# Kernel tuning notes

Measured on AMD Instinct MI355X. Metric: run time of the kernel, lower is better.

## Reference

```python
import jax, jax.numpy as jnp
import numpy as np
from jax import lax

K_SIZE = 3
STRIDE = 1
PADDING = 1


def setup_inputs() -> dict:
    key = jax.random.key(0)
    k1, k2, k3 = jax.random.split(key, 3)
    x = jax.random.normal(k1, (4, 64, 64, 256), dtype=jnp.float32)
    # small offsets so bilinear sampling stays near the regular grid (realistic DCN behavior)
    offset_w = jax.random.normal(k2, (3, 3, 256, 27), dtype=jnp.float32) * 0.01
    offset_b = jnp.zeros((1, 1, 1, 27), dtype=jnp.float32)
    dcn_weight = jax.random.normal(k3, (256, 256, 3, 3), dtype=jnp.float32) * 0.02
    return {"x": x, "offset_w": offset_w, "offset_b": offset_b, "dcn_weight": dcn_weight}


def _dcnv2(x, offset_w, offset_b, dcn_weight):
    k, stride, padding = K_SIZE, STRIDE, PADDING
    N, H, W, C = x.shape
    kk = k * k
    # offset/mask prediction conv (stride=1 -> SAME padding, per original code)
    om = lax.conv_general_dilated(
        x, offset_w, window_strides=(stride, stride), padding='SAME',
        dimension_numbers=('NHWC', 'HWIO', 'NHWC')) + offset_b
    offset = om[..., : 2 * kk]                      # [N,oH,oW,2k^2] (y,x) pairs
    mask = jax.nn.sigmoid(om[..., 2 * kk:])         # [N,oH,oW,k^2]
    oH = (H + 2 * padding - (k - 1)) // stride
    oW = (W + 2 * padding - (k - 1)) // stride
    # asymmetric zero padding ((p, p+1), (p, p+1)) as in the original
    pad_x = jnp.pad(x, ((0, 0), (padding, padding + 1), (padding, padding + 1), (0, 0)))
    # sampling grid: base center + fixed kernel offsets + learned offsets
    base_y = jnp.arange(oH, dtype=x.dtype) * stride + padding   # [oH]
    base_x = jnp.arange(oW, dtype=x.dtype) * stride + padding   # [oW]
    kr = jnp.arange(k, dtype=x.dtype) - (k - 1) / 2.0
    inner_y = jnp.repeat(kr, k)   # [k^2], row-major (kH, kW)
    inner_x = jnp.tile(kr, k)
    off_yx = offset.reshape(N, oH, oW, kk, 2)
    pos_y = base_y[None, :, None, None] + inner_y[None, None, None, :] + off_yx[..., 0]
    pos_x = base_x[None, None, :, None] + inner_x[None, None, None, :] + off_yx[..., 1]
    pos_y = jnp.clip(pos_y, 0.0, H + 2 * padding - 1.0)
    pos_x = jnp.clip(pos_x, 0.0, W + 2 * padding - 1.0)
    y1 = jnp.floor(pos_y)
    x1 = jnp.floor(pos_x)
    y1i = y1.astype(jnp.int32)
    x1i = x1.astype(jnp.int32)
    y2i = y1i + 1
    x2i = x1i + 1
    gather = jax.vmap(lambda px, yi, xi: px[yi, xi])  # per-sample [oH,oW,k^2] -> [oH,oW,k^2,C]
    v1 = gather(pad_x, y1i, x1i)
    v2 = gather(pad_x, y1i, x2i)
    v3 = gather(pad_x, y2i, x1i)
    v4 = gather(pad_x, y2i, x2i)
    lh = (pos_y - y1)[..., None]
    lw = (pos_x - x1)[..., None]
    hh = 1.0 - lh
    hw = 1.0 - lw
    value = (hh * hw * v1 + hh * lw * v2 + lh * hw * v3 + lh * lw * v4) * mask[..., None]
    # [N,oH,oW,k^2,C] -> [N,oH,oW,C,k^2] -> [N,oH,oW,C*k^2], matching original layout
    value = jnp.transpose(value, (0, 1, 2, 4, 3)).reshape(N, oH, oW, C * kk)
    w = jnp.transpose(dcn_weight, (1, 2, 3, 0)).reshape(C * kk, -1)  # [C*k^2, out_C]
    return jnp.einsum('nhwc,cf->nhwf', value, w)


def reference(x, offset_w, offset_b, dcn_weight):
    return _dcnv2(x, offset_w, offset_b, dcn_weight)
```

## Files before the change

kernel.cpp:

```cpp
#include <hip/hip_runtime.h>
#include <hip/hip_fp16.h>
#include <math.h>

typedef __attribute__((ext_vector_type(8))) _Float16 f16x8;
typedef __attribute__((ext_vector_type(4))) float f32x4;

#define XP_OFF   0
#define XP_BYTES (4*67*67*256*2)
#define WT_OFF   XP_BYTES
#define WT_BYTES (2304*256*2)
#define WOT_OFF  (WT_OFF + WT_BYTES)
#define WOT_BYTES (2304*32*2)
#define OM_OFF   (WOT_OFF + WOT_BYTES)
#define OM_BYTES (16384*32*4)
#define V_OFF    (OM_OFF + OM_BYTES)
#define V_BYTES  ((size_t)16384*2304*2)
#define WS_NEED  ((size_t)V_OFF + V_BYTES)

#define AS1(p) ((const __attribute__((address_space(1))) void*)(p))
#define AS3(p) ((__attribute__((address_space(3))) void*)(p))

__global__ __launch_bounds__(256) void prep_all(const float* __restrict__ x,
        const float* __restrict__ dw, const float* __restrict__ ow,
        __half* __restrict__ xp, __half* __restrict__ wt, __half* __restrict__ wot) {
    int b = blockIdx.x, tid = threadIdx.x;
    if (b < 2245) {
        int g = b * 256 + tid;
        if (g >= 17956 * 32) return;
        int row = g >> 5, sub = g & 31;
        int n = row / 4489, rem = row - n * 4489;
        int yy = rem / 67,  xx = rem - yy * 67;
        __half* dst = xp + (size_t)row * 256 + sub * 8;
        union { uint4 u; __half2 h[4]; } r;
        r.u = make_uint4(0u, 0u, 0u, 0u);
        if (yy >= 1 && yy <= 64 && xx >= 1 && xx <= 64) {
            const float* src = x + (((size_t)n * 64 + (yy - 1)) * 64 + (xx - 1)) * 256 + sub * 8;
            float4 a = *(const float4*)src;
            float4 c = *(const float4*)(src + 4);
            r.h[0] = __float22half2_rn(make_float2(a.x, a.y));
            r.h[1] = __float22half2_rn(make_float2(a.z, a.w));
            r.h[2] = __float22half2_rn(make_float2(c.x, c.y));
            r.h[3] = __float22half2_rn(make_float2(c.z, c.w));
        }
        *(uint4*)dst = r.u;
    } else if (b < 2501) {
        int oc = b - 2245, c = tid;
        const float* src = dw + oc * 2304 + c * 9;
        __half* dst = wt + oc * 2304 + c;
        #pragma unroll
        for (int t = 0; t < 9; ++t) dst[t * 256] = __float2half(src[t]);
    } else {
        int g = (b - 2501) * 256 + tid;
        int oc = g & 31, idx = g >> 5;
        float v = (oc < 27) ? ow[idx * 27 + oc] : 0.f;
        wot[oc * 2304 + idx] = __float2half(v);
    }
}

__global__ __launch_bounds__(256) void offset_mfma4(const __half* __restrict__ xp,
        const __half* __restrict__ wot, const float* __restrict__ ob,
        float* __restrict__ om) {
    __shared__ __align__(16) char sA[2][16384];
    int tid = threadIdx.x, lane = tid & 63, wave = tid >> 6;
    int bid = blockIdx.x;
    int mt = (bid & 7) * 64 + (bid >> 3);
    int p0 = mt * 32;
    int n = p0 >> 12, y = (p0 & 4095) >> 6, w0 = p0 & 63;
    const char* xpn = (const char*)(xp + (size_t)n * 4489 * 256);
    int wr = wave >> 1, wc = wave & 1;
    int ar = lane & 15, kl = (lane >> 4) * 8;

    int soff[4];
    #pragma unroll
    for (int q = 0; q < 4; ++q) {
        int d = (q * 256 + tid) * 16;
        int row = d >> 9;
        soff[q] = row * 512 + ((d & 511) ^ ((row & 7) << 4));
    }

    f32x4 acc = {0.f, 0.f, 0.f, 0.f};
    int r_a = wr * 16 + ar;
    int rsw = (r_a & 7) << 4;
    const __half* bb = wot + (size_t)(wc * 16 + ar) * 2304 + kl;

    #pragma unroll
    for (int q = 0; q < 4; ++q)
        __builtin_amdgcn_global_load_lds(AS1(xpn + ((y * 67 + w0) << 9) + soff[q]),
                                         AS3(&sA[0][(q * 256 + tid) * 16]), 16, 0, 0);
    __syncthreads();

    for (int t = 0; t < 9; ++t) {
        int buf = t & 1;
        if (t < 8) {
            int t1 = t + 1;
            int ty = t1 / 3, tx = t1 - 3 * ty;
            int sb = ((y + ty) * 67 + w0 + tx) << 9;
            #pragma unroll
            for (int q = 0; q < 4; ++q)
                __builtin_amdgcn_global_load_lds(AS1(xpn + sb + soff[q]),
                                                 AS3(&sA[buf ^ 1][(q * 256 + tid) * 16]), 16, 0, 0);
        }
        const __half* bp = bb + t * 256;
        #pragma unroll
        for (int c0 = 0; c0 < 256; c0 += 32) {
            f16x8 a = *(const f16x8*)(&sA[buf][0] + r_a * 512 + (((c0 + kl) * 2) ^ rsw));
            f16x8 bfr = *(const f16x8*)(bp + c0);
            acc = __builtin_amdgcn_mfma_f32_16x16x32_f16(a, bfr, acc, 0, 0, 0);
        }
        __syncthreads();
    }

    int col = wc * 16 + ar;
    float bias = (col < 27) ? ob[col] : 0.f;
    int rj = (lane >> 4) * 4;
    #pragma unroll
    for (int j = 0; j < 4; ++j)
        om[(size_t)(p0 + wr * 16 + rj + j) * 32 + col] = acc[j] + bias;
}

__global__ __launch_bounds__(256) void sample_v(const __half* __restrict__ xp,
        const float* __restrict__ om, __half* __restrict__ V) {
    int bid = blockIdx.x;
    int gb  = (bid & 7) * 2304 + (bid >> 3);
    int g = gb * 256 + threadIdx.x;
    int j = g >> 5;
    int s = g & 31;
    int p = j / 9;
    int t = j - p * 9;
    int n = p >> 12, y = (p >> 6) & 63, w = p & 63;
    const float* omp = om + (size_t)p * 32;
    float offy = omp[2 * t];
    float offx = omp[2 * t + 1];
    float mraw = omp[18 + t];
    float mask = 1.f / (1.f + __expf(-mraw));
    float py = (float)(y + 1) + (float)(t / 3 - 1) + offy;
    float px = (float)(w + 1) + (float)(t % 3 - 1) + offx;
    py = fminf(fmaxf(py, 0.f), 65.f);
    px = fminf(fmaxf(px, 0.f), 65.f);
    float y1f = floorf(py), x1f = floorf(px);
    int y1 = (int)y1f, x1 = (int)x1f;
    float ly = py - y1f, lx = px - x1f, hy = 1.f - ly, hx = 1.f - lx;
    const __half* b = xp + (size_t)n * 4489 * 256 + ((y1 * 67 + x1) << 8) + s * 8;
    union { uint4 u; __half2 h[4]; } cA, cB, cC, cD, r;
    cA.u = *(const uint4*)(b);
    cB.u = *(const uint4*)(b + 256);
    cC.u = *(const uint4*)(b + 17152);
    cD.u = *(const uint4*)(b + 17408);
    __half2 W11 = __float2half2_rn(hy * hx * mask), W12 = __float2half2_rn(hy * lx * mask);
    __half2 W21 = __float2half2_rn(ly * hx * mask), W22 = __float2half2_rn(ly * lx * mask);
    #pragma unroll
    for (int i = 0; i < 4; ++i)
        r.h[i] = __hfma2(cD.h[i], W22, __hfma2(cC.h[i], W21,
                 __hfma2(cB.h[i], W12, __hmul2(cA.h[i], W11))));
    *(uint4*)((char*)V + (size_t)g * 16) = r.u;
}

#define WAITVM(N) do { asm volatile("s_waitcnt vmcnt(" #N ")" ::: "memory"); \
                       __builtin_amdgcn_sched_barrier(0); } while (0)

#define STAGE_V4(BUF, KT) do { \
    _Pragma("unroll") \
    for (int q = 0; q < 2; ++q) \
        __builtin_amdgcn_global_load_lds(AS1(aS[q] + (size_t)(KT) * 128), \
            AS3(&sA[BUF][(q * 256 + tid) * 16]), 16, 0, 0); \
    _Pragma("unroll") \
    for (int q = 0; q < 4; ++q) \
        __builtin_amdgcn_global_load_lds(AS1(bS[q] + (size_t)(KT) * 128), \
            AS3(&sB[BUF][(q * 256 + tid) * 16]), 16, 0, 0); \
} while (0)

#define COMPUTE_V4(BUF) do { \
    _Pragma("unroll") \
    for (int kk = 0; kk < 2; ++kk) { \
        int ko = kk * 64 + kl * 2; \
        f16x8 af[2], bf[4]; \
        _Pragma("unroll") \
        for (int m = 0; m < 2; ++m) { \
            int r = wr * 32 + m * 16 + ar; \
            af[m] = *(const f16x8*)(&sA[BUF][0] + r * 128 + (ko ^ ((r & 7) << 4))); \
        } \
        _Pragma("unroll") \
        for (int nn = 0; nn < 4; ++nn) { \
            int r = wc * 64 + nn * 16 + ar; \
            bf[nn] = *(const f16x8*)(&sB[BUF][0] + r * 128 + (ko ^ ((r & 7) << 4))); \
        } \
        __builtin_amdgcn_s_setprio(1); \
        _Pragma("unroll") \
        for (int m = 0; m < 2; ++m) \
            _Pragma("unroll") \
            for (int nn = 0; nn < 4; ++nn) \
                acc[m][nn] = __builtin_amdgcn_mfma_f32_16x16x32_f16(af[m], bf[nn], acc[m][nn], 0, 0, 0); \
        __builtin_amdgcn_s_setprio(0); \
    } \
} while (0)

__global__ __launch_bounds__(256) void gemm_v4(const __half* __restrict__ V,
        const __half* __restrict__ wt, float* __restrict__ out) {
    __shared__ __align__(16) char sA[3][8192];
    __shared__ __align__(16) char sB[3][16384];
    int tid = threadIdx.x, lane = tid & 63, wave = tid >> 6;
    int bid = blockIdx.x;
    int xcd = bid & 7, idx = bid >> 3;
    int mt = xcd * 32 + (idx >> 1);
    int nt = idx & 1;
    int p0 = mt * 64, oc0 = nt * 128;
    int wr = wave >> 1, wc = wave & 1;
    int ar = lane & 15, kl = (lane >> 4) * 8;

    const char* aS[2]; const char* bS[4];
    #pragma unroll
    for (int q = 0; q < 2; ++q) {
        int d = (q * 256 + tid) * 16;
        int row = d >> 7, wb = d & 127;
        aS[q] = (const char*)V + (size_t)(p0 + row) * 4608 + (wb ^ ((row & 7) << 4));
    }
    #pragma unroll
    for (int q = 0; q < 4; ++q) {
        int d = (q * 256 + tid) * 16;
        int row = d >> 7, wb = d & 127;
        bS[q] = (const char*)wt + (size_t)(oc0 + row) * 4608 + (wb ^ ((row & 7) << 4));
    }

    f32x4 acc[2][4];
    #pragma unroll
    for (int m = 0; m < 2; ++m)
        #pragma unroll
        for (int nn = 0; nn < 4; ++nn) acc[m][nn] = (f32x4){0.f,0.f,0.f,0.f};

    STAGE_V4(0, 0);
    STAGE_V4(1, 1);
    STAGE_V4(2, 2);

    for (int kt = 0; kt < 34; ++kt) {
        int buf = kt % 3;
        WAITVM(12);
        __builtin_amdgcn_s_barrier();
        __builtin_amdgcn_sched_barrier(0);
        COMPUTE_V4(buf);
        __builtin_amdgcn_s_barrier();
        STAGE_V4(buf, kt + 3);
    }
    WAITVM(6);
    __builtin_amdgcn_s_barrier();
    __builtin_amdgcn_sched_barrier(0);
    COMPUTE_V4(34 % 3);
    __builtin_amdgcn_s_barrier();
    WAITVM(0);
    __builtin_amdgcn_s_barrier();
    __builtin_amdgcn_sched_barrier(0);
    COMPUTE_V4(35 % 3);

    int rj = (lane >> 4) * 4;
    #pragma unroll
    for (int m = 0; m < 2; ++m)
        #pragma unroll
        for (int nn = 0; nn < 4; ++nn)
            #pragma unroll
            for (int j = 0; j < 4; ++j)
                out[(size_t)(p0 + wr * 32 + m * 16 + rj + j) * 256 + oc0 + wc * 64 + nn * 16 + ar] = acc[m][nn][j];
}

__global__ __launch_bounds__(512) void dcn_mfma3(const __half* __restrict__ xp,
        const float* __restrict__ om, const __half* __restrict__ wt,
        float* __restrict__ out) {
    __shared__ char  s_v[16 * 512];
    __shared__ float s_ly[16][9], s_lx[16][9], s_m[16][9];
    __shared__ int   s_y1[16][9], s_x1[16][9];
    int tid  = threadIdx.x;
    int lane = tid & 63;
    int wave = tid >> 6;
    int bid  = blockIdx.x;
    int swzb = (bid & 7) * 128 + (bid >> 3);
    int p0 = swzb * 16;
    int n  = p0 >> 12;
    int y  = (p0 & 4095) >> 6;
    int w0 = p0 & 63;
    const __half* xpn = xp + (size_t)n * 4489 * 256;
    if (tid < 144) {
        int ps = tid / 9, k = tid - 9 * ps;
        int p  = p0 + ps;
        float offy = om[(size_t)p * 32 + 2 * k];
        float offx = om[(size_t)p * 32 + 2 * k + 1];
        float mraw = om[(size_t)p * 32 + 18 + k];
        float mask = 1.f / (1.f + __expf(-mraw));
        float py = (float)(y + 1)       + (float)(k / 3 - 1) + offy;
        float px = (float)(w0 + ps + 1) + (float)(k % 3 - 1) + offx;
        py = fminf(fmaxf(py, 0.f), 65.f);
        px = fminf(fmaxf(px, 0.f), 65.f);
        float y1f = floorf(py), x1f = floorf(px);
        s_y1[ps][k] = (int)y1f;
        s_x1[ps][k] = (int)x1f;
        s_ly[ps][k] = py - y1f;
        s_lx[ps][k] = px - x1f;
        s_m [ps][k] = mask;
    }
    __syncthreads();
    int px = tid >> 5;
    int ch = (tid & 31) * 8;
    int ar = lane & 15;
    int kl = (lane >> 4) * 8;
    int oc0 = wave * 32;
    const __half* bp0 = wt + (size_t)(oc0 + ar) * 2304 + kl;
    const __half* bp1 = wt + (size_t)(oc0 + 16 + ar) * 2304 + kl;
    int wr_off = px * 512 + (((tid & 31) * 16) ^ ((px & 7) << 4));
    int rd_row = ar * 512;
    int rd_swz = (ar & 7) << 4;
    f32x4 acc0 = {0.f,0.f,0.f,0.f}, acc1 = {0.f,0.f,0.f,0.f};
    for (int t = 0; t < 9; ++t) {
        int y1 = s_y1[px][t], x1 = s_x1[px][t];
        const __half* b = xpn + ((size_t)(y1 * 67 + x1) << 8) + ch;
        union { uint4 u; __half2 h[4]; } cA, cB, cC, cD, r;
        cA.u = *(const uint4*)(b);
        cB.u = *(const uint4*)(b + 256);
        cC.u = *(const uint4*)(b + 17152);
        cD.u = *(const uint4*)(b + 17408);
        float ly = s_ly[px][t], lx = s_lx[px][t], mk = s_m[px][t];
        float hy = 1.f - ly, hx = 1.f - lx;
        __half2 W11 = __float2half2_rn(hy * hx * mk);
        __half2 W12 = __float2half2_rn(hy * lx * mk);
        __half2 W21 = __float2half2_rn(ly * hx * mk);
        __half2 W22 = __float2half2_rn(ly * lx * mk);
        #pragma unroll
        for (int i = 0; i < 4; ++i)
            r.h[i] = __hfma2(cD.h[i], W22, __hfma2(cC.h[i], W21,
                     __hfma2(cB.h[i], W12, __hmul2(cA.h[i], W11))));
        *(uint4*)(s_v + wr_off) = r.u;
        __syncthreads();
        const __half* b0 = bp0 + t * 256;
        const __half* b1 = bp1 + t * 256;
        #pragma unroll
        for (int c0 = 0; c0 < 256; c0 += 32) {
            f16x8 a   = *(const f16x8*)(s_v + rd_row + (((c0 + kl) * 2) ^ rd_swz));
            f16x8 vb0 = *(const f16x8*)(b0 + c0);
            f16x8 vb1 = *(const f16x8*)(b1 + c0);
            acc0 = __builtin_amdgcn_mfma_f32_16x16x32_f16(a, vb0, acc0, 0, 0, 0);
            acc1 = __builtin_amdgcn_mfma_f32_16x16x32_f16(a, vb1, acc1, 0, 0, 0);
        }
        __syncthreads();
    }
    int rj = (lane >> 4) * 4;
    #pragma unroll
    for (int j = 0; j < 4; ++j) {
        out[(size_t)(p0 + rj + j) * 256 + oc0 + ar]      = acc0[j];
        out[(size_t)(p0 + rj + j) * 256 + oc0 + 16 + ar] = acc1[j];
    }
}

extern "C" void kernel_launch(void* const* d_in, const int* in_sizes, int n_in,
                              void* d_out, int out_size, void* d_ws, size_t ws_size,
                              hipStream_t stream) {
    const float* x  = (const float*)d_in[0];
    const float* ow = (const float*)d_in[1];
    const float* ob = (const float*)d_in[2];
    const float* dw = (const float*)d_in[3];
    __half* xpp = (__half*)((char*)d_ws + XP_OFF);
    __half* wt  = (__half*)((char*)d_ws + WT_OFF);
    __half* wot = (__half*)((char*)d_ws + WOT_OFF);
    float*  omp = (float*)((char*)d_ws + OM_OFF);
    __half* Vp  = (__half*)((char*)d_ws + V_OFF);
    float* out = (float*)d_out;

    hipLaunchKernelGGL(prep_all,     dim3(2789), dim3(256), 0, stream, x, dw, ow, xpp, wt, wot);
    hipLaunchKernelGGL(offset_mfma4, dim3(512),  dim3(256), 0, stream, xpp, wot, ob, omp);
    if (ws_size >= WS_NEED) {
        hipLaunchKernelGGL(sample_v, dim3(18432), dim3(256), 0, stream, xpp, omp, Vp);
        hipLaunchKernelGGL(gemm_v4,  dim3(512),   dim3(256), 0, stream, Vp, wt, out);
    } else {
        hipLaunchKernelGGL(dcn_mfma3, dim3(1024), dim3(512), 0, stream, xpp, omp, wt, out);
    }
}
```

Measured before the change: 81.33 us.

## Enlarge GEMM block tile to 128x128 with 512 threads and 4-stage pipeline

Replaces the 64x128 GEMM tile per 256-thread block with a 128x128 tile per 512-thread block (8 waves), halving the block count to 256. Each output tile now reuses its loaded weight slice across twice as many rows, so less global and L2 traffic is spent per flop. The LDS ring deepens from 3 to 4 stages, using 128KB of LDS. In exchange there is one block per CU and fewer blocks overall, which may reduce latency hiding and load balance.

```diff
diff --git a/kernel.cpp b/kernel.cpp
--- a/kernel.cpp
+++ b/kernel.cpp
@@ -158,18 +158,18 @@
 #define WAITVM(N) do { asm volatile("s_waitcnt vmcnt(" #N ")" ::: "memory"); \
                        __builtin_amdgcn_sched_barrier(0); } while (0)
 
-#define STAGE_V4(BUF, KT) do { \
+#define STAGE_V5(BUF, KT) do { \
     _Pragma("unroll") \
     for (int q = 0; q < 2; ++q) \
         __builtin_amdgcn_global_load_lds(AS1(aS[q] + (size_t)(KT) * 128), \
-            AS3(&sA[BUF][(q * 256 + tid) * 16]), 16, 0, 0); \
+            AS3(&sA[BUF][(q * 512 + tid) * 16]), 16, 0, 0); \
     _Pragma("unroll") \
-    for (int q = 0; q < 4; ++q) \
+    for (int q = 0; q < 2; ++q) \
         __builtin_amdgcn_global_load_lds(AS1(bS[q] + (size_t)(KT) * 128), \
-            AS3(&sB[BUF][(q * 256 + tid) * 16]), 16, 0, 0); \
+            AS3(&sB[BUF][(q * 512 + tid) * 16]), 16, 0, 0); \
 } while (0)
 
-#define COMPUTE_V4(BUF) do { \
+#define COMPUTE_V5(BUF) do { \
     _Pragma("unroll") \
     for (int kk = 0; kk < 2; ++kk) { \
         int ko = kk * 64 + kl * 2; \
@@ -194,30 +194,32 @@
     } \
 } while (0)
 
-__global__ __launch_bounds__(256) void gemm_v4(const __half* __restrict__ V,
+#define TAIL_V5(N, BUF) do { \
+    WAITVM(N); \
+    __builtin_amdgcn_s_barrier(); \
+    __builtin_amdgcn_sched_barrier(0); \
+    COMPUTE_V5(BUF); \
+} while (0)
+
+__global__ __launch_bounds__(512) void gemm_v5(const __half* __restrict__ V,
         const __half* __restrict__ wt, float* __restrict__ out) {
-    __shared__ __align__(16) char sA[3][8192];
-    __shared__ __align__(16) char sB[3][16384];
+    __shared__ __align__(16) char sA[4][16384];
+    __shared__ __align__(16) char sB[4][16384];
     int tid = threadIdx.x, lane = tid & 63, wave = tid >> 6;
     int bid = blockIdx.x;
     int xcd = bid & 7, idx = bid >> 3;
-    int mt = xcd * 32 + (idx >> 1);
+    int mt = xcd * 16 + (idx >> 1);
     int nt = idx & 1;
-    int p0 = mt * 64, oc0 = nt * 128;
+    int p0 = mt * 128, oc0 = nt * 128;
     int wr = wave >> 1, wc = wave & 1;
     int ar = lane & 15, kl = (lane >> 4) * 8;
 
-    const char* aS[2]; const char* bS[4];
+    const char* aS[2]; const char* bS[2];
     #pragma unroll
     for (int q = 0; q < 2; ++q) {
-        int d = (q * 256 + tid) * 16;
+        int d = (q * 512 + tid) * 16;
         int row = d >> 7, wb = d & 127;
-        aS[q] = (const char*)V + (size_t)(p0 + row) * 4608 + (wb ^ ((row & 7) << 4));
-    }
-    #pragma unroll
-    for (int q = 0; q < 4; ++q) {
-        int d = (q * 256 + tid) * 16;
-        int row = d >> 7, wb = d & 127;
+        aS[q] = (const char*)V  + (size_t)(p0  + row) * 4608 + (wb ^ ((row & 7) << 4));
         bS[q] = (const char*)wt + (size_t)(oc0 + row) * 4608 + (wb ^ ((row & 7) << 4));
     }
 
@@ -227,28 +229,27 @@
         #pragma unroll
         for (int nn = 0; nn < 4; ++nn) acc[m][nn] = (f32x4){0.f,0.f,0.f,0.f};
 
-    STAGE_V4(0, 0);
-    STAGE_V4(1, 1);
-    STAGE_V4(2, 2);
-
-    for (int kt = 0; kt < 34; ++kt) {
-        int buf = kt % 3;
+    STAGE_V5(0, 0);
+    STAGE_V5(1, 1);
+    STAGE_V5(2, 2);
+    STAGE_V5(3, 3);
+
+    for (int kt = 0; kt < 32; ++kt) {
+        int buf = kt & 3;
         WAITVM(12);
         __builtin_amdgcn_s_barrier();
         __builtin_amdgcn_sched_barrier(0);
-        COMPUTE_V4(buf);
+        COMPUTE_V5(buf);
         __builtin_amdgcn_s_barrier();
-        STAGE_V4(buf, kt + 3);
-    }
-    WAITVM(6);
+        STAGE_V5(buf, kt + 4);
+    }
+    TAIL_V5(12, 0);
     __builtin_amdgcn_s_barrier();
-    __builtin_amdgcn_sched_barrier(0);
-    COMPUTE_V4(34 % 3);
+    TAIL_V5(8, 1);
     __builtin_amdgcn_s_barrier();
-    WAITVM(0);
+    TAIL_V5(4, 2);
     __builtin_amdgcn_s_barrier();
-    __builtin_amdgcn_sched_barrier(0);
-    COMPUTE_V4(35 % 3);
+    TAIL_V5(0, 3);
 
     int rj = (lane >> 4) * 4;
     #pragma unroll
@@ -364,7 +365,7 @@
     hipLaunchKernelGGL(offset_mfma4, dim3(512),  dim3(256), 0, stream, xpp, wot, ob, omp);
     if (ws_size >= WS_NEED) {
         hipLaunchKernelGGL(sample_v, dim3(18432), dim3(256), 0, stream, xpp, omp, Vp);
-        hipLaunchKernelGGL(gemm_v4,  dim3(512),   dim3(256), 0, stream, Vp, wt, out);
+        hipLaunchKernelGGL(gemm_v5,  dim3(256),   dim3(512), 0, stream, Vp, wt, out);
     } else {
         hipLaunchKernelGGL(dcn_mfma3, dim3(1024), dim3(512), 0, stream, xpp, omp, wt, out);
     }
```

Result: slower. 85.36 us (+5.0%).
